# Optimization experiments

Hardware: AMD Instinct MI355X
Metric: run time of the kernel (lower is better)

## Reference

```python
import jax, jax.numpy as jnp
import numpy as np

DIM = 128
HEADS = 4
WIN = 7
N = WIN * WIN
B_ = 4096
NW = 64


def _relative_position_index():
    coords = np.stack(np.meshgrid(np.arange(WIN), np.arange(WIN), indexing='ij'))  # [2,W,W]
    flat = coords.reshape(2, -1)  # [2, N]
    rel = flat[:, :, None] - flat[:, None, :]  # [2, N, N]
    rel = rel.transpose(1, 2, 0)  # [N, N, 2]
    rel[:, :, 0] += WIN - 1
    rel[:, :, 1] += WIN - 1
    rel[:, :, 0] *= 2 * WIN - 1
    return rel.sum(-1).astype(np.int32)  # [N, N], values in [0, (2W-1)^2)


def setup_inputs() -> dict:
    key = jax.random.key(0)
    ks = jax.random.split(key, 12)
    s = 0.02
    inp = {
        'query': jax.random.normal(ks[0], (B_, N, DIM), jnp.float32),
        'key': jax.random.normal(ks[1], (B_, N, DIM), jnp.float32),
        'value': jax.random.normal(ks[2], (B_, N, DIM), jnp.float32),
        'Wq': jax.random.normal(ks[3], (DIM, DIM), jnp.float32) * s,
        'bq': jnp.zeros((DIM,), jnp.float32),
        'Wk': jax.random.normal(ks[4], (DIM, DIM), jnp.float32) * s,
        'bk': jnp.zeros((DIM,), jnp.float32),
        'Wv': jax.random.normal(ks[5], (DIM, DIM), jnp.float32) * s,
        'bv': jnp.zeros((DIM,), jnp.float32),
        'bias_table': jax.random.normal(ks[6], ((2 * WIN - 1) ** 2, HEADS), jnp.float32) * s,
        'Wp': jax.random.normal(ks[7], (DIM, DIM), jnp.float32) * s,
        'bp': jnp.zeros((DIM,), jnp.float32),
        # Swin-style shift mask: 0 or -100 per window pair (here random 0/-100 pattern)
        'mask': jnp.where(jax.random.uniform(ks[8], (NW, N, N)) < 0.8, 0.0, -100.0).astype(jnp.float32),
        'rel_index': jnp.asarray(_relative_position_index()),
    }
    return inp


def reference(query, key, value, Wq, bq, Wk, bk, Wv, bv, bias_table, Wp, bp, mask, rel_index):
    Bw, n, C = query.shape
    H = HEADS
    hd = C // H
    scale = hd ** (-0.5)
    # projections (torch Linear: x @ W^T + b), split heads -> [B_, H, N, hd]
    q = (query @ Wq.T + bq).reshape(Bw, n, H, hd).transpose(0, 2, 1, 3)
    k = (key @ Wk.T + bk).reshape(Bw, n, H, hd).transpose(0, 2, 1, 3)
    v = (value @ Wv.T + bv).reshape(Bw, n, H, hd).transpose(0, 2, 1, 3)
    attn = jnp.einsum('bhnd,bhmd->bhnm', q * scale, k)  # [B_, H, N, N]
    rel_bias = bias_table[rel_index]  # [N, N, H]
    attn = attn + rel_bias.transpose(2, 0, 1)[None]
    nW = mask.shape[0]
    attn = attn.reshape(Bw // nW, nW, H, n, n) + mask[None, :, None]
    attn = attn.reshape(Bw, H, n, n)
    attn = jax.nn.softmax(attn, axis=-1)
    x = jnp.einsum('bhnm,bhmd->bhnd', attn, v).transpose(0, 2, 1, 3).reshape(Bw, n, C)
    return x @ Wp.T + bp
```

## Files before the change

### kernel.cpp

```cpp
#include <hip/hip_runtime.h>
#include <hip/hip_bf16.h>

#define DIMC 128
#define HD   32
#define NTOK 49
#define SSTR 136
#define VSTR 72

#define OFF_K      17408
#define OFF_VT     34816
#define SMEM_BYTES 53248

#define WS_WFRAG   1024
#define WS_ADDB    (1024 + 131072)
#define WS_BIAS    (1024 + 131072 + 4194304)

using bf16x8 = __attribute__((ext_vector_type(8))) __bf16;
using u16x8  = __attribute__((ext_vector_type(8))) ushort;
using f32x4  = __attribute__((ext_vector_type(4))) float;

static __device__ __forceinline__ ushort f2b(float f) {
  __hip_bfloat16 h = __float2bfloat16(f);
  return __builtin_bit_cast(ushort, h);
}
static __device__ __forceinline__ float b2f(ushort u) {
  __hip_bfloat16 h = __builtin_bit_cast(__hip_bfloat16, u);
  return __bfloat162float(h);
}
static __device__ __forceinline__ float scrub(float v, float lim) {
  return fminf(fmaxf(v, -lim), lim);
}
static __device__ __forceinline__ float ldany(const void* p, int i, int isbf) {
  return isbf ? b2f(((const ushort*)p)[i]) : ((const float*)p)[i];
}

__global__ void detect_dtype_kernel(const ushort* __restrict__ q, int* __restrict__ flag) {
  if (threadIdx.x == 0 && blockIdx.x == 0) {
    int c = 0;
    for (int i = 0; i < 256; ++i) {
      int e = (q[i] >> 7) & 0xFF;
      c += (e >= 110 && e <= 133) ? 1 : 0;
    }
    *flag = (c >= 200) ? 1 : 0;
  }
}

__global__ __launch_bounds__(256) void prep_kernel(
    const void* __restrict__ Wq, const void* __restrict__ Wk,
    const void* __restrict__ Wv, const void* __restrict__ Wp,
    const void* __restrict__ bq, const void* __restrict__ bk,
    const void* __restrict__ bv, const void* __restrict__ bp,
    const void* __restrict__ btab, const void* __restrict__ gmask,
    const int* __restrict__ relidx,
    ushort* __restrict__ wfrag, float* __restrict__ addb, float* __restrict__ biasf,
    const int* __restrict__ flag)
{
  const int isbf = *flag;
  const int gtid = blockIdx.x * 256 + threadIdx.x;
  const int gstr = gridDim.x * 256;
  const void* Ws[4] = {Wq, Wk, Wv, Wp};
  const void* bs[4] = {bq, bk, bv, bp};

  for (int i = gtid; i < 4 * 16384; i += gstr) {
    int mat = i >> 14;
    int nt  = (i >> 11) & 7;
    int k   = (i >> 9) & 3;
    int ln  = (i >> 3) & 63;
    int j   = i & 7;
    int row = nt * 16 + (ln & 15);
    int col = k * 32 + (ln >> 4) * 8 + j;
    wfrag[i] = f2b(ldany(Ws[mat], row * DIMC + col, isbf));
  }
  for (int i = gtid; i < 512; i += gstr)
    biasf[i] = ldany(bs[i >> 7], i & 127, isbf);

  for (int i = gtid; i < 64 * 4 * 16 * 64 * 4; i += gstr) {
    int r  = i & 3;
    int ln = (i >> 2) & 63;
    int rc = (i >> 8) & 15;
    int h  = (i >> 12) & 3;
    int wi = i >> 14;
    int rt = rc >> 2, ct = rc & 3;
    int n = rt * 16 + (ln >> 4) * 4 + r;
    int m = ct * 16 + (ln & 15);
    float v;
    if (n >= NTOK || m >= NTOK) {
      v = -30000.f;
    } else {
      int ri = relidx[n * NTOK + m];
      v = ldany(btab, ri * 4 + h, isbf) + ldany(gmask, (wi * NTOK + n) * NTOK + m, isbf);
    }
    addb[i] = v;
  }
}

__global__ __launch_bounds__(256, 3) void swin_attn_kernel(
    const void* __restrict__ gq, const void* __restrict__ gk, const void* __restrict__ gv,
    const ushort* __restrict__ wfrag, const float* __restrict__ addb,
    const float* __restrict__ biasf,
    void* __restrict__ goutv, const int* __restrict__ flag)
{
  __shared__ __align__(16) char smem[SMEM_BYTES];
  ushort* sQ  = (ushort*)smem;
  ushort* sK  = (ushort*)(smem + OFF_K);
  ushort* sVt = (ushort*)(smem + OFF_VT);

  const int b    = blockIdx.x;
  const int tid  = threadIdx.x;
  const int wave = tid >> 6;
  const int lane = tid & 63;
  const int quad = lane >> 4;
  const int l16  = lane & 15;
  const int wi   = b & 63;
  const int isbf = *flag;
  const int h    = wave, koff = h * HD;
  const int n0a  = wave * 32, n0b = n0a + 16;

  auto ldxfrag = [&](const void* src, int row, int col) -> bf16x8 {
    u16x8 u = {0, 0, 0, 0, 0, 0, 0, 0};
    if (row < NTOK) {
      if (isbf) {
        const ushort* s = (const ushort*)src + (size_t)b * NTOK * DIMC + row * DIMC + col;
        u = *(const u16x8*)s;
      } else {
        const float* s = (const float*)src + (size_t)b * NTOK * DIMC + row * DIMC + col;
        float4 f0 = *(const float4*)s;
        float4 f1 = *(const float4*)(s + 4);
        u[0] = f2b(f0.x); u[1] = f2b(f0.y); u[2] = f2b(f0.z); u[3] = f2b(f0.w);
        u[4] = f2b(f1.x); u[5] = f2b(f1.y); u[6] = f2b(f1.z); u[7] = f2b(f1.w);
      }
    }
    return __builtin_bit_cast(bf16x8, u);
  };

  auto proj = [&](const void* src, int mat, int p) {
    const ushort* wb = wfrag + mat * 16384;
    bf16x8 bfr[2][4];
#pragma unroll
    for (int k = 0; k < 4; ++k) {
      bfr[0][k] = *(const bf16x8*)&wb[(((n0a >> 4) * 4) + k) * 512 + lane * 8];
      bfr[1][k] = *(const bf16x8*)&wb[(((n0b >> 4) * 4) + k) * 512 + lane * 8];
    }
    const float b0 = biasf[mat * 128 + n0a + l16];
    const float b1 = biasf[mat * 128 + n0b + l16];
#pragma unroll
    for (int mt = 0; mt < 4; ++mt) {
      bf16x8 af[4];
#pragma unroll
      for (int k = 0; k < 4; ++k)
        af[k] = ldxfrag(src, mt * 16 + l16, k * 32 + quad * 8);
      f32x4 a0 = {0.f, 0.f, 0.f, 0.f}, a1 = {0.f, 0.f, 0.f, 0.f};
#pragma unroll
      for (int k = 0; k < 4; ++k) {
        a0 = __builtin_amdgcn_mfma_f32_16x16x32_bf16(af[k], bfr[0][k], a0, 0, 0, 0);
        a1 = __builtin_amdgcn_mfma_f32_16x16x32_bf16(af[k], bfr[1][k], a1, 0, 0, 0);
      }
      if (p == 2) {
        ushort4 pk;
        pk.x = f2b(scrub(a0[0] + b0, 30000.f)); pk.y = f2b(scrub(a0[1] + b0, 30000.f));
        pk.z = f2b(scrub(a0[2] + b0, 30000.f)); pk.w = f2b(scrub(a0[3] + b0, 30000.f));
        *(ushort4*)&sVt[(n0a + l16) * VSTR + mt * 16 + quad * 4] = pk;
        pk.x = f2b(scrub(a1[0] + b1, 30000.f)); pk.y = f2b(scrub(a1[1] + b1, 30000.f));
        pk.z = f2b(scrub(a1[2] + b1, 30000.f)); pk.w = f2b(scrub(a1[3] + b1, 30000.f));
        *(ushort4*)&sVt[(n0b + l16) * VSTR + mt * 16 + quad * 4] = pk;
      } else {
        ushort* dst = p ? sK : sQ;
#pragma unroll
        for (int r = 0; r < 4; ++r) {
          int row = mt * 16 + quad * 4 + r;
          float bb0 = (row < NTOK) ? b0 : 0.f;
          float bb1 = (row < NTOK) ? b1 : 0.f;
          dst[row * SSTR + n0a + l16] = f2b(scrub(a0[r] + bb0, 30000.f));
          dst[row * SSTR + n0b + l16] = f2b(scrub(a1[r] + bb1, 30000.f));
        }
      }
    }
  };

  proj(gq, 0, 0);
  proj(gk, 1, 1);
  proj(gv, 2, 2);

  bf16x8 qa[4], kb[4];
#pragma unroll
  for (int t = 0; t < 4; ++t) {
    qa[t] = *(const bf16x8*)&sQ[(t * 16 + l16) * SSTR + koff + quad * 8];
    kb[t] = *(const bf16x8*)&sK[(t * 16 + l16) * SSTR + koff + quad * 8];
  }
  __syncthreads();

  f32x4 s[4][4];
#pragma unroll
  for (int rt = 0; rt < 4; ++rt)
#pragma unroll
    for (int ct = 0; ct < 4; ++ct) {
      f32x4 z = {0.f, 0.f, 0.f, 0.f};
      s[rt][ct] = __builtin_amdgcn_mfma_f32_16x16x32_bf16(qa[rt], kb[ct], z, 0, 0, 0);
    }

  const float scale = 0.17677669529663687f;
  const float* ab = addb + (size_t)(wi * 4 + h) * 16 * 256 + lane * 4;
#pragma unroll
  for (int rt = 0; rt < 4; ++rt) {
#pragma unroll
    for (int ct = 0; ct < 4; ++ct) {
      f32x4 a4 = *(const f32x4*)(ab + (rt * 4 + ct) * 256);
#pragma unroll
      for (int r = 0; r < 4; ++r)
        s[rt][ct][r] = scrub(s[rt][ct][r] * scale + a4[r], 30000.f);
    }
#pragma unroll
    for (int r = 0; r < 4; ++r) {
      float m0 = fmaxf(fmaxf(s[rt][0][r], s[rt][1][r]), fmaxf(s[rt][2][r], s[rt][3][r]));
      m0 = fmaxf(m0, __shfl_xor(m0, 1));
      m0 = fmaxf(m0, __shfl_xor(m0, 2));
      m0 = fmaxf(m0, __shfl_xor(m0, 4));
      m0 = fmaxf(m0, __shfl_xor(m0, 8));
      float t0 = 0.f;
#pragma unroll
      for (int ct = 0; ct < 4; ++ct) {
        float e = __expf(s[rt][ct][r] - m0);
        s[rt][ct][r] = e;
        t0 += e;
      }
      t0 += __shfl_xor(t0, 1);
      t0 += __shfl_xor(t0, 2);
      t0 += __shfl_xor(t0, 4);
      t0 += __shfl_xor(t0, 8);
      float inv = 1.0f / fmaxf(t0, 1e-20f);
#pragma unroll
      for (int ct = 0; ct < 4; ++ct) s[rt][ct][r] *= inv;
    }
  }

  ushort* sP = sQ + wave * 1152;
  bf16x8 pa[4][2];
#pragma unroll
  for (int rt = 0; rt < 4; ++rt) {
#pragma unroll
    for (int ct = 0; ct < 4; ++ct)
#pragma unroll
      for (int r = 0; r < 4; ++r)
        sP[(quad * 4 + r) * VSTR + ct * 16 + l16] = f2b(s[rt][ct][r]);
#pragma unroll
    for (int ks = 0; ks < 2; ++ks)
      pa[rt][ks] = *(const bf16x8*)&sP[l16 * VSTR + ks * 32 + quad * 8];
  }

  bf16x8 vb[2][2];
#pragma unroll
  for (int ct = 0; ct < 2; ++ct)
#pragma unroll
    for (int ks = 0; ks < 2; ++ks)
      vb[ct][ks] = *(const bf16x8*)&sVt[(koff + ct * 16 + l16) * VSTR + ks * 32 + quad * 8];
  f32x4 xacc[4][2];
#pragma unroll
  for (int rt = 0; rt < 4; ++rt)
#pragma unroll
    for (int ct = 0; ct < 2; ++ct) {
      f32x4 z = {0.f, 0.f, 0.f, 0.f};
      z = __builtin_amdgcn_mfma_f32_16x16x32_bf16(pa[rt][0], vb[ct][0], z, 0, 0, 0);
      xacc[rt][ct] = __builtin_amdgcn_mfma_f32_16x16x32_bf16(pa[rt][1], vb[ct][1], z, 0, 0, 0);
    }
  __syncthreads();

  ushort* sXp = sQ;
#pragma unroll
  for (int rt = 0; rt < 4; ++rt)
#pragma unroll
    for (int ct = 0; ct < 2; ++ct)
#pragma unroll
      for (int r = 0; r < 4; ++r) {
        int row = rt * 16 + quad * 4 + r;
        sXp[row * SSTR + koff + ct * 16 + l16] = f2b(scrub(xacc[rt][ct][r], 1e4f));
      }
  __syncthreads();

  {
    const ushort* wb = wfrag + 3 * 16384;
    bf16x8 wf[2][4];
#pragma unroll
    for (int k = 0; k < 4; ++k) {
      wf[0][k] = *(const bf16x8*)&wb[(((n0a >> 4) * 4) + k) * 512 + lane * 8];
      wf[1][k] = *(const bf16x8*)&wb[(((n0b >> 4) * 4) + k) * 512 + lane * 8];
    }
    const float bo0 = biasf[3 * 128 + n0a + l16];
    const float bo1 = biasf[3 * 128 + n0b + l16];
#pragma unroll
    for (int mt = 0; mt < 4; ++mt) {
      bf16x8 af[4];
#pragma unroll
      for (int k = 0; k < 4; ++k)
        af[k] = *(const bf16x8*)&sXp[(mt * 16 + l16) * SSTR + k * 32 + quad * 8];
      f32x4 a0 = {0.f, 0.f, 0.f, 0.f}, a1 = {0.f, 0.f, 0.f, 0.f};
#pragma unroll
      for (int k = 0; k < 4; ++k) {
        a0 = __builtin_amdgcn_mfma_f32_16x16x32_bf16(af[k], wf[0][k], a0, 0, 0, 0);
        a1 = __builtin_amdgcn_mfma_f32_16x16x32_bf16(af[k], wf[1][k], a1, 0, 0, 0);
      }
#pragma unroll
      for (int r = 0; r < 4; ++r) {
        int row = mt * 16 + quad * 4 + r;
        if (row < NTOK) {
          size_t o = (size_t)(b * NTOK + row) * DIMC;
          float v0 = scrub(a0[r] + bo0, 1e4f);
          float v1 = scrub(a1[r] + bo1, 1e4f);
          if (isbf) {
            ((__hip_bfloat16*)goutv)[o + n0a + l16] = __float2bfloat16(v0);
            ((__hip_bfloat16*)goutv)[o + n0b + l16] = __float2bfloat16(v1);
          } else {
            ((float*)goutv)[o + n0a + l16] = v0;
            ((float*)goutv)[o + n0b + l16] = v1;
          }
        }
      }
    }
  }
}

extern "C" void kernel_launch(void* const* d_in, const int* in_sizes, int n_in,
                              void* d_out, int out_size, void* d_ws, size_t ws_size,
                              hipStream_t stream) {
  const int B = in_sizes[0] / (NTOK * DIMC);
  int* flag = (int*)d_ws;
  ushort* wfrag = (ushort*)((char*)d_ws + WS_WFRAG);
  float* addb = (float*)((char*)d_ws + WS_ADDB);
  float* biasf = (float*)((char*)d_ws + WS_BIAS);
  detect_dtype_kernel<<<1, 64, 0, stream>>>((const ushort*)d_in[0], flag);
  prep_kernel<<<512, 256, 0, stream>>>(
      d_in[3], d_in[5], d_in[7], d_in[10],
      d_in[4], d_in[6], d_in[8], d_in[11],
      d_in[9], d_in[12], (const int*)d_in[13],
      wfrag, addb, biasf, flag);
  swin_attn_kernel<<<B, 256, 0, stream>>>(
      d_in[0], d_in[1], d_in[2], wfrag, addb, biasf, d_out, flag);
}
```

Measured before the change: 520.3 us.

## Shrink shared memory to fit four blocks per CU and restructure softmax per row

```diff
diff --git a/kernel.cpp b/kernel.cpp
--- a/kernel.cpp
+++ b/kernel.cpp
@@ -5,11 +5,12 @@
 #define HD   32
 #define NTOK 49
 #define SSTR 136
-#define VSTR 72
-
-#define OFF_K      17408
-#define OFF_VT     34816
-#define SMEM_BYTES 53248
+#define PSTR 72
+#define VTSTR 52
+
+#define OFF_K      13328
+#define OFF_VT     26656
+#define SMEM_BYTES 40000
 
 #define WS_WFRAG   1024
 #define WS_ADDB    (1024 + 131072)
@@ -94,7 +95,7 @@
   }
 }
 
-__global__ __launch_bounds__(256, 3) void swin_attn_kernel(
+__global__ __launch_bounds__(256, 4) void swin_attn_kernel(
     const void* __restrict__ gq, const void* __restrict__ gk, const void* __restrict__ gv,
     const ushort* __restrict__ wfrag, const float* __restrict__ addb,
     const float* __restrict__ biasf,
@@ -115,6 +116,8 @@
   const int isbf = *flag;
   const int h    = wave, koff = h * HD;
   const int n0a  = wave * 32, n0b = n0a + 16;
+
+  if (tid < 2) ((int4*)(smem + OFF_VT + 13312))[tid] = make_int4(0, 0, 0, 0);
 
   auto ldxfrag = [&](const void* src, int row, int col) -> bf16x8 {
     u16x8 u = {0, 0, 0, 0, 0, 0, 0, 0};
@@ -156,22 +159,24 @@
         a1 = __builtin_amdgcn_mfma_f32_16x16x32_bf16(af[k], bfr[1][k], a1, 0, 0, 0);
       }
       if (p == 2) {
-        ushort4 pk;
-        pk.x = f2b(scrub(a0[0] + b0, 30000.f)); pk.y = f2b(scrub(a0[1] + b0, 30000.f));
-        pk.z = f2b(scrub(a0[2] + b0, 30000.f)); pk.w = f2b(scrub(a0[3] + b0, 30000.f));
-        *(ushort4*)&sVt[(n0a + l16) * VSTR + mt * 16 + quad * 4] = pk;
-        pk.x = f2b(scrub(a1[0] + b1, 30000.f)); pk.y = f2b(scrub(a1[1] + b1, 30000.f));
-        pk.z = f2b(scrub(a1[2] + b1, 30000.f)); pk.w = f2b(scrub(a1[3] + b1, 30000.f));
-        *(ushort4*)&sVt[(n0b + l16) * VSTR + mt * 16 + quad * 4] = pk;
+        if (mt < 3 || quad == 0) {
+          ushort4 pk;
+          pk.x = f2b(scrub(a0[0] + b0, 30000.f)); pk.y = f2b(scrub(a0[1] + b0, 30000.f));
+          pk.z = f2b(scrub(a0[2] + b0, 30000.f)); pk.w = f2b(scrub(a0[3] + b0, 30000.f));
+          *(ushort4*)&sVt[(n0a + l16) * VTSTR + mt * 16 + quad * 4] = pk;
+          pk.x = f2b(scrub(a1[0] + b1, 30000.f)); pk.y = f2b(scrub(a1[1] + b1, 30000.f));
+          pk.z = f2b(scrub(a1[2] + b1, 30000.f)); pk.w = f2b(scrub(a1[3] + b1, 30000.f));
+          *(ushort4*)&sVt[(n0b + l16) * VTSTR + mt * 16 + quad * 4] = pk;
+        }
       } else {
         ushort* dst = p ? sK : sQ;
 #pragma unroll
         for (int r = 0; r < 4; ++r) {
           int row = mt * 16 + quad * 4 + r;
-          float bb0 = (row < NTOK) ? b0 : 0.f;
-          float bb1 = (row < NTOK) ? b1 : 0.f;
-          dst[row * SSTR + n0a + l16] = f2b(scrub(a0[r] + bb0, 30000.f));
-          dst[row * SSTR + n0b + l16] = f2b(scrub(a1[r] + bb1, 30000.f));
+          if (row < NTOK) {
+            dst[row * SSTR + n0a + l16] = f2b(scrub(a0[r] + b0, 30000.f));
+            dst[row * SSTR + n0b + l16] = f2b(scrub(a1[r] + b1, 30000.f));
+          }
         }
       }
     }
@@ -187,31 +192,37 @@
     qa[t] = *(const bf16x8*)&sQ[(t * 16 + l16) * SSTR + koff + quad * 8];
     kb[t] = *(const bf16x8*)&sK[(t * 16 + l16) * SSTR + koff + quad * 8];
   }
+  {
+    const u16x8 z8 = {0, 0, 0, 0, 0, 0, 0, 0};
+    if (l16 != 0) {
+      qa[3] = __builtin_bit_cast(bf16x8, z8);
+      kb[3] = __builtin_bit_cast(bf16x8, z8);
+    }
+  }
   __syncthreads();
 
-  f32x4 s[4][4];
-#pragma unroll
-  for (int rt = 0; rt < 4; ++rt)
+  const float scale = 0.17677669529663687f;
+  const float* ab = addb + (size_t)(wi * 4 + h) * 16 * 256 + lane * 4;
+  ushort* sP = sQ + wave * 1152;
+  bf16x8 pa[4][2];
+#pragma unroll
+  for (int rt = 0; rt < 4; ++rt) {
+    f32x4 srow[4];
 #pragma unroll
     for (int ct = 0; ct < 4; ++ct) {
       f32x4 z = {0.f, 0.f, 0.f, 0.f};
-      s[rt][ct] = __builtin_amdgcn_mfma_f32_16x16x32_bf16(qa[rt], kb[ct], z, 0, 0, 0);
-    }
-
-  const float scale = 0.17677669529663687f;
-  const float* ab = addb + (size_t)(wi * 4 + h) * 16 * 256 + lane * 4;
-#pragma unroll
-  for (int rt = 0; rt < 4; ++rt) {
+      srow[ct] = __builtin_amdgcn_mfma_f32_16x16x32_bf16(qa[rt], kb[ct], z, 0, 0, 0);
+    }
 #pragma unroll
     for (int ct = 0; ct < 4; ++ct) {
       f32x4 a4 = *(const f32x4*)(ab + (rt * 4 + ct) * 256);
 #pragma unroll
       for (int r = 0; r < 4; ++r)
-        s[rt][ct][r] = scrub(s[rt][ct][r] * scale + a4[r], 30000.f);
+        srow[ct][r] = scrub(srow[ct][r] * scale + a4[r], 30000.f);
     }
 #pragma unroll
     for (int r = 0; r < 4; ++r) {
-      float m0 = fmaxf(fmaxf(s[rt][0][r], s[rt][1][r]), fmaxf(s[rt][2][r], s[rt][3][r]));
+      float m0 = fmaxf(fmaxf(srow[0][r], srow[1][r]), fmaxf(srow[2][r], srow[3][r]));
       m0 = fmaxf(m0, __shfl_xor(m0, 1));
       m0 = fmaxf(m0, __shfl_xor(m0, 2));
       m0 = fmaxf(m0, __shfl_xor(m0, 4));
@@ -219,8 +230,8 @@
       float t0 = 0.f;
 #pragma unroll
       for (int ct = 0; ct < 4; ++ct) {
-        float e = __expf(s[rt][ct][r] - m0);
-        s[rt][ct][r] = e;
+        float e = __expf(srow[ct][r] - m0);
+        srow[ct][r] = e;
         t0 += e;
       }
       t0 += __shfl_xor(t0, 1);
@@ -229,30 +240,31 @@
       t0 += __shfl_xor(t0, 8);
       float inv = 1.0f / fmaxf(t0, 1e-20f);
 #pragma unroll
-      for (int ct = 0; ct < 4; ++ct) s[rt][ct][r] *= inv;
-    }
-  }
-
-  ushort* sP = sQ + wave * 1152;
-  bf16x8 pa[4][2];
-#pragma unroll
-  for (int rt = 0; rt < 4; ++rt) {
+      for (int ct = 0; ct < 4; ++ct) srow[ct][r] *= inv;
+    }
 #pragma unroll
     for (int ct = 0; ct < 4; ++ct)
 #pragma unroll
       for (int r = 0; r < 4; ++r)
-        sP[(quad * 4 + r) * VSTR + ct * 16 + l16] = f2b(s[rt][ct][r]);
+        sP[(quad * 4 + r) * PSTR + ct * 16 + l16] = f2b(srow[ct][r]);
 #pragma unroll
     for (int ks = 0; ks < 2; ++ks)
-      pa[rt][ks] = *(const bf16x8*)&sP[l16 * VSTR + ks * 32 + quad * 8];
-  }
-
+      pa[rt][ks] = *(const bf16x8*)&sP[l16 * PSTR + ks * 32 + quad * 8];
+  }
+
+  auto ldvt = [&](int rowf, int colt) -> bf16x8 {
+    const ushort* p = &sVt[rowf * VTSTR + colt];
+    ushort4 lo = *(const ushort4*)p;
+    ushort4 hi = *(const ushort4*)(p + 4);
+    u16x8 u = {lo.x, lo.y, lo.z, lo.w, hi.x, hi.y, hi.z, hi.w};
+    return __builtin_bit_cast(bf16x8, u);
+  };
   bf16x8 vb[2][2];
 #pragma unroll
   for (int ct = 0; ct < 2; ++ct)
 #pragma unroll
     for (int ks = 0; ks < 2; ++ks)
-      vb[ct][ks] = *(const bf16x8*)&sVt[(koff + ct * 16 + l16) * VSTR + ks * 32 + quad * 8];
+      vb[ct][ks] = ldvt(koff + ct * 16 + l16, ks * 32 + quad * 8);
   f32x4 xacc[4][2];
 #pragma unroll
   for (int rt = 0; rt < 4; ++rt)
@@ -262,30 +274,35 @@
       z = __builtin_amdgcn_mfma_f32_16x16x32_bf16(pa[rt][0], vb[ct][0], z, 0, 0, 0);
       xacc[rt][ct] = __builtin_amdgcn_mfma_f32_16x16x32_bf16(pa[rt][1], vb[ct][1], z, 0, 0, 0);
     }
-  __syncthreads();
-
-  ushort* sXp = sQ;
-#pragma unroll
-  for (int rt = 0; rt < 4; ++rt)
-#pragma unroll
-    for (int ct = 0; ct < 2; ++ct)
-#pragma unroll
-      for (int r = 0; r < 4; ++r) {
-        int row = rt * 16 + quad * 4 + r;
-        sXp[row * SSTR + koff + ct * 16 + l16] = f2b(scrub(xacc[rt][ct][r], 1e4f));
-      }
-  __syncthreads();
-
+
+  bf16x8 wf[2][4];
   {
     const ushort* wb = wfrag + 3 * 16384;
-    bf16x8 wf[2][4];
 #pragma unroll
     for (int k = 0; k < 4; ++k) {
       wf[0][k] = *(const bf16x8*)&wb[(((n0a >> 4) * 4) + k) * 512 + lane * 8];
       wf[1][k] = *(const bf16x8*)&wb[(((n0b >> 4) * 4) + k) * 512 + lane * 8];
     }
+  }
+  __syncthreads();
+
+  ushort* sXp = sQ;
+#pragma unroll
+  for (int rt = 0; rt < 4; ++rt)
+#pragma unroll
+    for (int ct = 0; ct < 2; ++ct)
+#pragma unroll
+      for (int r = 0; r < 4; ++r) {
+        int row = rt * 16 + quad * 4 + r;
+        if (row < NTOK)
+          sXp[row * SSTR + koff + ct * 16 + l16] = f2b(scrub(xacc[rt][ct][r], 1e4f));
+      }
+  __syncthreads();
+
+  {
     const float bo0 = biasf[3 * 128 + n0a + l16];
     const float bo1 = biasf[3 * 128 + n0b + l16];
+    ushort* sOut = sK;
 #pragma unroll
     for (int mt = 0; mt < 4; ++mt) {
       bf16x8 af[4];
@@ -302,17 +319,25 @@
       for (int r = 0; r < 4; ++r) {
         int row = mt * 16 + quad * 4 + r;
         if (row < NTOK) {
-          size_t o = (size_t)(b * NTOK + row) * DIMC;
           float v0 = scrub(a0[r] + bo0, 1e4f);
           float v1 = scrub(a1[r] + bo1, 1e4f);
           if (isbf) {
-            ((__hip_bfloat16*)goutv)[o + n0a + l16] = __float2bfloat16(v0);
-            ((__hip_bfloat16*)goutv)[o + n0b + l16] = __float2bfloat16(v1);
+            sOut[row * SSTR + n0a + l16] = f2b(v0);
+            sOut[row * SSTR + n0b + l16] = f2b(v1);
           } else {
+            size_t o = (size_t)(b * NTOK + row) * DIMC;
             ((float*)goutv)[o + n0a + l16] = v0;
             ((float*)goutv)[o + n0b + l16] = v1;
           }
         }
+      }
+    }
+    if (isbf) {
+      __syncthreads();
+      ushort* gout = (ushort*)goutv + (size_t)b * NTOK * DIMC;
+      for (int c = tid; c < NTOK * 16; c += 256) {
+        int row = c >> 4, j = c & 15;
+        *(int4*)&gout[row * DIMC + j * 8] = *(const int4*)&sOut[row * SSTR + j * 8];
       }
     }
   }
```

Result: faster. 461.4 us (-11.3%).
